# Kernel optimization log

Hardware: AMD Instinct MI355X
Metric: run time of the kernel (lower is better)

## Reference

```python
import jax, jax.numpy as jnp
import numpy as np

N = 50_000        # nodes
E = 1_600_000     # edges (avg degree 32)
H = 64            # hidden_channels
DEPTH = 3         # -> 2*DEPTH mid conv layers


def setup_inputs() -> dict:
    key = jax.random.key(0)
    ks = jax.random.split(key, 8)
    x = jax.random.normal(ks[0], (N, 1), dtype=jnp.float32)
    edge_index = jax.random.randint(ks[1], (2, E), 0, N, dtype=jnp.int32)
    s = 0.1  # small init scale
    W_in = s * jax.random.normal(ks[2], (2 * 1 + 1, H), dtype=jnp.float32)
    b_in = jnp.zeros((H,), jnp.float32)
    W_mid = s * jax.random.normal(ks[3], (2 * DEPTH, 2 * H + 1, H), dtype=jnp.float32)
    b_mid = jnp.zeros((2 * DEPTH, H), jnp.float32)
    W_out = s * jax.random.normal(ks[4], (2 * H + 1, 1), dtype=jnp.float32)
    b_out = jnp.zeros((1,), jnp.float32)
    return {"x": x, "edge_index": edge_index, "W_in": W_in, "b_in": b_in,
            "W_mid": W_mid, "b_mid": b_mid, "W_out": W_out, "b_out": b_out}


def _conv(x, src, dst, sign, inv_deg, W, b):
    """Directional_EdgeConv: mean_{j->i} Linear([x_i, x_j - x_i, sign(j-i)])."""
    x_i = x[dst]                                   # [E, F] target feats
    x_j = x[src]                                   # [E, F] source feats
    feat = jnp.concatenate([x_i, x_j - x_i, sign], axis=-1)  # [E, 2F+1]
    msg = feat @ W + b                             # [E, out]
    agg = jax.ops.segment_sum(msg, dst, num_segments=x.shape[0])  # [N, out]
    return agg * inv_deg                           # mean aggregation


def reference(x, edge_index, W_in, b_in, W_mid, b_mid, W_out, b_out):
    src = edge_index[0]
    dst = edge_index[1]
    # vectorized replacement of the per-edge Python sign loop
    sign = jnp.sign((src - dst).astype(x.dtype))[:, None]        # [E, 1]
    deg = jax.ops.segment_sum(jnp.ones((src.shape[0],), x.dtype), dst,
                              num_segments=x.shape[0])
    inv_deg = (1.0 / jnp.maximum(deg, 1.0))[:, None]             # [N, 1]

    x2 = _conv(x, src, dst, sign, inv_deg, W_in, b_in)
    for l in range(DEPTH):
        x1 = jax.nn.leaky_relu(
            _conv(x2, src, dst, sign, inv_deg, W_mid[2 * l], b_mid[2 * l]))
        x2 = jax.nn.leaky_relu(
            _conv(x1, src, dst, sign, inv_deg, W_mid[2 * l + 1], b_mid[2 * l + 1]) + x2)
    return _conv(x2, src, dst, sign, inv_deg, W_out, b_out) + x
```

## Files before the change

### kernel.cpp

```cpp
#include <hip/hip_runtime.h>
#include <hip/hip_fp16.h>

#define HDIM 64
#define NEG_SLOPE 0.01f
#define CAPB 8192
#define BCAP 6144

typedef _Float16 half8 __attribute__((ext_vector_type(8)));
typedef float f32x4 __attribute__((ext_vector_type(4)));

static __device__ __forceinline__ float h_lo(unsigned d) {
    return __half2float(__ushort_as_half((unsigned short)(d & 0xffffu)));
}
static __device__ __forceinline__ float h_hi(unsigned d) {
    return __half2float(__ushort_as_half((unsigned short)(d >> 16)));
}
static __device__ __forceinline__ unsigned packh(float a, float b) {
    unsigned short ra = __half_as_ushort(__float2half(a));
    unsigned short rb = __half_as_ushort(__float2half(b));
    return ((unsigned)rb << 16) | (unsigned)ra;
}
static __device__ __forceinline__ half8 u4h(uint4 v) {
    union { uint4 u; half8 h; } x; x.u = v; return x.h;
}
static __device__ __forceinline__ __half2 uh2(unsigned u) {
    union { unsigned u; __half2 h; } x; x.u = u; return x.h;
}

__global__ void k_setup(int ptotal, const float* __restrict__ W_mid,
                        unsigned short* __restrict__ WTh,
                        int NB, int* gcur, int N, unsigned* xAP, unsigned* xBP) {
    int i = blockIdx.x * blockDim.x + threadIdx.x;
    if (i < ptotal) {
        int l = i >> 13;
        int rem = i & 8191;
        int h = rem >> 7;
        int k = rem & 127;
        const float* W = W_mid + (size_t)l * 129 * 64;
        float v = W[k * 64 + h] - ((k < 64) ? W[(64 + k) * 64 + h] : 0.f);
        WTh[i] = __half_as_ushort(__float2half(v));
    }
    if (i < NB) gcur[i] = i * CAPB;
    if (i < 32) xAP[(size_t)N * 32 + i] = 0u;
    else if (i < 64) xBP[(size_t)N * 32 + (i - 32)] = 0u;
}

__global__ __launch_bounds__(1024) void k_bucket(
        int E, const int* __restrict__ src, const int* __restrict__ dst,
        int* gcur, unsigned* __restrict__ bucketed, int NB) {
    __shared__ int lh[512];
    __shared__ int lbase[512];
    int t = threadIdx.x;
    int e0 = blockIdx.x * 2048;
    if (t < 512) lh[t] = 0;
    __syncthreads();
    int e1 = e0 + t, e2 = e0 + 1024 + t;
    int d1 = (e1 < E) ? dst[e1] : -1;
    int d2 = (e2 < E) ? dst[e2] : -1;
    if (d1 >= 0) atomicAdd(&lh[((unsigned)d1) >> 7], 1);
    if (d2 >= 0) atomicAdd(&lh[((unsigned)d2) >> 7], 1);
    __syncthreads();
    if (t < NB) {
        int c = lh[t];
        lbase[t] = (c > 0) ? atomicAdd(&gcur[t], c) : 0;
        lh[t] = 0;
    }
    __syncthreads();
    int s1 = (e1 < E) ? src[e1] : 0;
    int s2 = (e2 < E) ? src[e2] : 0;
    if (d1 >= 0) {
        int b = ((unsigned)d1) >> 7;
        int r = atomicAdd(&lh[b], 1);
        int pos = lbase[b] + r;
        if (pos < (b + 1) * CAPB)
            bucketed[pos] = ((unsigned)d1 << 16) | (unsigned)s1;
    }
    if (d2 >= 0) {
        int b = ((unsigned)d2) >> 7;
        int r = atomicAdd(&lh[b], 1);
        int pos = lbase[b] + r;
        if (pos < (b + 1) * CAPB)
            bucketed[pos] = ((unsigned)d2 << 16) | (unsigned)s2;
    }
}

__global__ void k_bktscan(int NB, int N, const int* __restrict__ gcur,
                          int* gstart, int* rowptr) {
    __shared__ int sd[512];
    int t = threadIdx.x;
    int c = (t < NB) ? min(gcur[t] - t * CAPB, CAPB) : 0;
    sd[t] = c;
    __syncthreads();
    int x = c;
    for (int s = 1; s < 512; s <<= 1) {
        int p = (t >= s) ? sd[t - s] : 0;
        __syncthreads();
        x += p;
        sd[t] = x;
        __syncthreads();
    }
    if (t < NB) gstart[t] = x - c;
    if (t == NB - 1) {
        gstart[NB] = x;
        rowptr[N] = x;
    }
}

__global__ void k_csr(int N, const unsigned* __restrict__ bucketed, const int* __restrict__ gcur,
                      const int* __restrict__ gstart, unsigned short* __restrict__ csr,
                      unsigned short* __restrict__ pcsr,
                      int* __restrict__ rowptr, float* __restrict__ ssinv) {
    __shared__ unsigned st[BCAP];
    __shared__ int hist[128], cur[128], excl[128], sgp[128];
    int b = blockIdx.x, t = threadIdx.x;
    int n0 = b << 7;
    int nn = min(128, N - n0);
    int cnt = min(gcur[b] - b * CAPB, CAPB);
    int base = gstart[b];
    if (t < 128) { hist[t] = 0; sgp[t] = 0; }
    unsigned sent = ((unsigned)N << 16) | (unsigned)N;
    unsigned* pb32 = (unsigned*)(pcsr + ((size_t)b << 13));
    for (int i = t; i < 4096; i += 256) pb32[i] = sent;
    __syncthreads();
    bool single = (cnt <= BCAP);
    for (int off = 0; off < cnt; off += BCAP) {
        int bs = min(BCAP, cnt - off);
        for (int i = t; i < bs; i += 256) {
            unsigned w = bucketed[b * CAPB + off + i];
            if (single) st[i] = w;
            int d = (int)(w >> 16);
            int s = (int)(w & 0xffffu);
            int dl = d - n0;
            atomicAdd(&hist[dl], 1);
            atomicAdd(&sgp[dl], ((s < d) ? 1024 : 0) + ((s == d) ? 1 : 0));
        }
    }
    __syncthreads();
    int deg_t = (t < 128) ? hist[t] : 0;
    int x = deg_t;
    for (int s = 1; s < 128; s <<= 1) {
        int p = (t < 128 && t >= s) ? hist[t - s] : 0;
        __syncthreads();
        if (t < 128) { x += p; hist[t] = x; }
        __syncthreads();
    }
    if (t < 128) {
        int ex = hist[t] - deg_t;
        excl[t] = ex;
        cur[t] = ex;
        if (t < nn) {
            rowptr[n0 + t] = base + ex;
            int sg = sgp[t];
            int lt = sg >> 10, eq = sg & 1023;
            float ss = (float)(deg_t - eq - 2 * lt);
            ssinv[n0 + t] = (deg_t > 0) ? ss / (float)deg_t : 0.f;
        }
    }
    __syncthreads();
    for (int off = 0; off < cnt; off += BCAP) {
        int bs = min(BCAP, cnt - off);
        if (!single) {
            for (int i = t; i < bs; i += 256) st[i] = bucketed[b * CAPB + off + i];
            __syncthreads();
        }
        for (int i = t; i < bs; i += 256) {
            unsigned w = st[i];
            int dl = (int)(w >> 16) - n0;
            unsigned short sval = (unsigned short)(w & 0xffffu);
            int p = atomicAdd(&cur[dl], 1);
            csr[base + p] = sval;
            int r = p - excl[dl];
            if (r < 64) pcsr[((size_t)(n0 + dl) << 6) + r] = sval;
        }
        if (!single) __syncthreads();
    }
}

__global__ void k_in(int N, const float* __restrict__ x0,
                     const int* __restrict__ rowptr, const unsigned short* __restrict__ csr,
                     const float* __restrict__ ssinv,
                     const float* __restrict__ W_in, const float* __restrict__ b_in,
                     unsigned* __restrict__ xoutP) {
    int wid = blockIdx.x * (blockDim.x >> 6) + (threadIdx.x >> 6);
    int lane = threadIdx.x & 63;
    if (wid >= N) return;
    int beg = rowptr[wid], end = rowptr[wid + 1];
    int deg = end - beg;
    float s = 0.f;
    for (int e = beg + lane; e < end; e += 64) s += x0[csr[e]];
    for (int m = 32; m >= 1; m >>= 1) s += __shfl_xor(s, m, 64);
    float invd = 1.f / (float)max(deg, 1);
    float mean = s * invd;
    float xi = x0[wid];
    float w1 = W_in[lane], w2 = W_in[64 + lane], w3 = W_in[128 + lane];
    float y = xi * (w1 - w2) + mean * w2 + ssinv[wid] * w3 + b_in[lane];
    if (deg == 0) y = 0.f;
    float ylo = __shfl(y, (2 * lane) & 63, 64);
    float yhi = __shfl(y, (2 * lane + 1) & 63, 64);
    unsigned pkd = packh(ylo, yhi);
    if (lane < 32) xoutP[(size_t)wid * 32 + lane] = pkd;
}

static __device__ __forceinline__ void chunk_acc(
        const uint4* __restrict__ xin16, int sv, int base, int sub, int lq,
        __half2& c0, __half2& c1, __half2& c2, __half2& c3) {
    int s0 = __shfl(sv, base + sub, 64);
    int s1 = __shfl(sv, base + 8 + sub, 64);
    int s2 = __shfl(sv, base + 16 + sub, 64);
    int s3 = __shfl(sv, base + 24 + sub, 64);
    uint4 d0 = xin16[(size_t)s0 * 8 + lq];
    uint4 d1 = xin16[(size_t)s1 * 8 + lq];
    uint4 d2 = xin16[(size_t)s2 * 8 + lq];
    uint4 d3 = xin16[(size_t)s3 * 8 + lq];
    c0 = __hadd2(c0, __hadd2(__hadd2(uh2(d0.x), uh2(d1.x)), __hadd2(uh2(d2.x), uh2(d3.x))));
    c1 = __hadd2(c1, __hadd2(__hadd2(uh2(d0.y), uh2(d1.y)), __hadd2(uh2(d2.y), uh2(d3.y))));
    c2 = __hadd2(c2, __hadd2(__hadd2(uh2(d0.z), uh2(d1.z)), __hadd2(uh2(d2.z), uh2(d3.z))));
    c3 = __hadd2(c3, __hadd2(__hadd2(uh2(d0.w), uh2(d1.w)), __hadd2(uh2(d2.w), uh2(d3.w))));
}

static __device__ __forceinline__ void slow_gather(
        const uint4* __restrict__ xin16, const unsigned short* __restrict__ csr,
        int beg, int end, int N, int lane, int sub, int lq, float* a) {
#pragma unroll
    for (int j = 0; j < 8; ++j) a[j] = 0.f;
    for (int tb = beg; tb < end; tb += 64) {
        int cnt = min(64, end - tb);
        int sv = (lane < cnt) ? (int)csr[tb + lane] : N;
        int ng = (cnt + 7) >> 3;
        for (int g = 0; g < ng; ++g) {
            int si = __shfl(sv, (g << 3) + sub, 64);
            uint4 d = xin16[(size_t)si * 8 + lq];
            a[0] += h_lo(d.x); a[1] += h_hi(d.x);
            a[2] += h_lo(d.y); a[3] += h_hi(d.y);
            a[4] += h_lo(d.z); a[5] += h_hi(d.z);
            a[6] += h_lo(d.w); a[7] += h_hi(d.w);
        }
    }
#pragma unroll
    for (int m = 8; m <= 32; m <<= 1) {
#pragma unroll
        for (int j = 0; j < 8; ++j) a[j] += __shfl_xor(a[j], m, 64);
    }
}

template <bool RES, bool TOUT>
__global__ __launch_bounds__(256) void k_layer(
        int N, const unsigned* __restrict__ xinP,
        const unsigned* __restrict__ xresP, unsigned* __restrict__ xoutP,
        const int* __restrict__ rowptr, const unsigned short* __restrict__ csr,
        const unsigned short* __restrict__ pcsr,
        const float* __restrict__ ssinv,
        const unsigned short* __restrict__ WThl,
        const float* __restrict__ W3, const float* __restrict__ bias,
        const float* __restrict__ Wt, float* __restrict__ tvec) {
    __shared__ unsigned Ald[16 * 64];
    __shared__ float Cld[16 * 64];
    __shared__ int sdeg[16];
    __shared__ float sss[16];

    int t = threadIdx.x;
    int lane = t & 63;
    int wv = t >> 6;
    int n0 = blockIdx.x << 4;
    int kg = lane >> 4;

    int cb = (wv << 4) + (lane & 15);
    const uint4* wp = (const uint4*)WThl;
    uint4 b0 = wp[cb * 16 + kg + 0];
    uint4 b1 = wp[cb * 16 + kg + 4];
    uint4 b2 = wp[cb * 16 + kg + 8];
    uint4 b3 = wp[cb * 16 + kg + 12];

    const uint4* xin16 = (const uint4*)xinP;
    int sub = lane >> 3;
    int lq = lane & 7;
    int ndb = wv << 2;

    int svp[4];
#pragma unroll
    for (int q = 0; q < 4; ++q)
        svp[q] = (int)pcsr[((size_t)(n0 + ndb + q) << 6) + lane];

#pragma unroll
    for (int qp = 0; qp < 2; ++qp) {
        int ndA = ndb + (qp << 1);
        int ndB = ndA + 1;
        int nodeA = n0 + ndA, nodeB = n0 + ndB;
        int ncA = min(nodeA, N - 1), ncB = min(nodeB, N - 1);
        int begA = __builtin_amdgcn_readfirstlane(rowptr[ncA]);
        int endA = __builtin_amdgcn_readfirstlane(rowptr[ncA + 1]);
        int begB = __builtin_amdgcn_readfirstlane(rowptr[ncB]);
        int endB = __builtin_amdgcn_readfirstlane(rowptr[ncB + 1]);
        int degA = (nodeA < N) ? (endA - begA) : 0;
        int degB = (nodeB < N) ? (endB - begB) : 0;
        float ssvA = ssinv[ncA];
        float ssvB = ssinv[ncB];
        uint4 xiA = make_uint4(0u, 0u, 0u, 0u), xiB = make_uint4(0u, 0u, 0u, 0u);
        if (lane < 8) {
            xiA = xin16[(size_t)ncA * 8 + lane];
            xiB = xin16[(size_t)ncB * 8 + lane];
        }
        uint4 mvA, mvB;
        if (max(degA, degB) <= 64) {
            __half2 z = uh2(0u);
            __half2 cA0 = z, cA1 = z, cA2 = z, cA3 = z;
            __half2 cB0 = z, cB1 = z, cB2 = z, cB3 = z;
            int svA = svp[qp << 1], svB = svp[(qp << 1) + 1];
            chunk_acc(xin16, svA, 0, sub, lq, cA0, cA1, cA2, cA3);
            chunk_acc(xin16, svB, 0, sub, lq, cB0, cB1, cB2, cB3);
            if (degA > 32) chunk_acc(xin16, svA, 32, sub, lq, cA0, cA1, cA2, cA3);
            if (degB > 32) chunk_acc(xin16, svB, 32, sub, lq, cB0, cB1, cB2, cB3);
#pragma unroll
            for (int m = 8; m <= 32; m <<= 1) {
                cA0 = __hadd2(cA0, uh2((unsigned)__shfl_xor((int)*(unsigned*)&cA0, m, 64)));
                cA1 = __hadd2(cA1, uh2((unsigned)__shfl_xor((int)*(unsigned*)&cA1, m, 64)));
                cA2 = __hadd2(cA2, uh2((unsigned)__shfl_xor((int)*(unsigned*)&cA2, m, 64)));
                cA3 = __hadd2(cA3, uh2((unsigned)__shfl_xor((int)*(unsigned*)&cA3, m, 64)));
                cB0 = __hadd2(cB0, uh2((unsigned)__shfl_xor((int)*(unsigned*)&cB0, m, 64)));
                cB1 = __hadd2(cB1, uh2((unsigned)__shfl_xor((int)*(unsigned*)&cB1, m, 64)));
                cB2 = __hadd2(cB2, uh2((unsigned)__shfl_xor((int)*(unsigned*)&cB2, m, 64)));
                cB3 = __hadd2(cB3, uh2((unsigned)__shfl_xor((int)*(unsigned*)&cB3, m, 64)));
            }
            float idA = 1.f / (float)max(degA, 1);
            float idB = 1.f / (float)max(degB, 1);
            mvA.x = packh(__half2float(__low2half(cA0)) * idA, __half2float(__high2half(cA0)) * idA);
            mvA.y = packh(__half2float(__low2half(cA1)) * idA, __half2float(__high2half(cA1)) * idA);
            mvA.z = packh(__half2float(__low2half(cA2)) * idA, __half2float(__high2half(cA2)) * idA);
            mvA.w = packh(__half2float(__low2half(cA3)) * idA, __half2float(__high2half(cA3)) * idA);
            mvB.x = packh(__half2float(__low2half(cB0)) * idB, __half2float(__high2half(cB0)) * idB);
            mvB.y = packh(__half2float(__low2half(cB1)) * idB, __half2float(__high2half(cB1)) * idB);
            mvB.z = packh(__half2float(__low2half(cB2)) * idB, __half2float(__high2half(cB2)) * idB);
            mvB.w = packh(__half2float(__low2half(cB3)) * idB, __half2float(__high2half(cB3)) * idB);
        } else {
            float aA[8], aB[8];
            slow_gather(xin16, csr, begA, endA, N, lane, sub, lq, aA);
            slow_gather(xin16, csr, begB, endB, N, lane, sub, lq, aB);
            float idA = 1.f / (float)max(degA, 1);
            float idB = 1.f / (float)max(degB, 1);
            mvA.x = packh(aA[0] * idA, aA[1] * idA);
            mvA.y = packh(aA[2] * idA, aA[3] * idA);
            mvA.z = packh(aA[4] * idA, aA[5] * idA);
            mvA.w = packh(aA[6] * idA, aA[7] * idA);
            mvB.x = packh(aB[0] * idB, aB[1] * idB);
            mvB.y = packh(aB[2] * idB, aB[3] * idB);
            mvB.z = packh(aB[4] * idB, aB[5] * idB);
            mvB.w = packh(aB[6] * idB, aB[7] * idB);
        }
        if (lane < 8) {
            int gxA = lane ^ (ndA & 7), gmA = (8 + lane) ^ (ndA & 7);
            int gxB = lane ^ (ndB & 7), gmB = (8 + lane) ^ (ndB & 7);
            ((uint4*)Ald)[ndA * 16 + gxA] = xiA;
            ((uint4*)Ald)[ndA * 16 + gmA] = mvA;
            ((uint4*)Ald)[ndB * 16 + gxB] = xiB;
            ((uint4*)Ald)[ndB * 16 + gmB] = mvB;
        }
        if (lane == 0) {
            sdeg[ndA] = degA; sss[ndA] = ssvA;
            sdeg[ndB] = degB; sss[ndB] = ssvB;
        }
    }
    __syncthreads();

    int r = lane & 15;
    const uint4* ap = (const uint4*)Ald;
    int rx = (r & 7);
    uint4 fa0 = ap[r * 16 + ((0 + kg) ^ rx)];
    uint4 fa1 = ap[r * 16 + ((4 + kg) ^ rx)];
    uint4 fa2 = ap[r * 16 + ((8 + kg) ^ rx)];
    uint4 fa3 = ap[r * 16 + ((12 + kg) ^ rx)];
    f32x4 acc = {0.f, 0.f, 0.f, 0.f};
    acc = __builtin_amdgcn_mfma_f32_16x16x32_f16(u4h(fa0), u4h(b0), acc, 0, 0, 0);
    acc = __builtin_amdgcn_mfma_f32_16x16x32_f16(u4h(fa1), u4h(b1), acc, 0, 0, 0);
    acc = __builtin_amdgcn_mfma_f32_16x16x32_f16(u4h(fa2), u4h(b2), acc, 0, 0, 0);
    acc = __builtin_amdgcn_mfma_f32_16x16x32_f16(u4h(fa3), u4h(b3), acc, 0, 0, 0);
#pragma unroll
    for (int reg = 0; reg < 4; ++reg)
        Cld[(kg * 4 + reg) * 64 + (wv << 4) + r] = acc[reg];
    __syncthreads();

    int nd = t >> 4;
    int node = n0 + nd;
    if (node < N) {
        int dg = sdeg[nd];
        float ss = sss[nd];
        float tp = 0.f;
#pragma unroll
        for (int jj = 0; jj < 2; ++jj) {
            int j = (t & 15) + jj * 16;
            float y0 = Cld[nd * 64 + 2 * j];
            float y1 = Cld[nd * 64 + 2 * j + 1];
            float2 w3 = ((const float2*)W3)[j];
            float2 bb = ((const float2*)bias)[j];
            y0 += ss * w3.x + bb.x;
            y1 += ss * w3.y + bb.y;
            if (dg == 0) { y0 = 0.f; y1 = 0.f; }
            if (RES) {
                unsigned rw = xresP[(size_t)node * 32 + j];
                y0 += h_lo(rw);
                y1 += h_hi(rw);
            }
            y0 = (y0 > 0.f) ? y0 : NEG_SLOPE * y0;
            y1 = (y1 > 0.f) ? y1 : NEG_SLOPE * y1;
            if (TOUT) {
                float2 wt = ((const float2*)Wt)[j];
                tp += y0 * wt.x + y1 * wt.y;
            }
            xoutP[(size_t)node * 32 + j] = packh(y0, y1);
        }
        if (TOUT) {
            tp += __shfl_xor(tp, 1, 64);
            tp += __shfl_xor(tp, 2, 64);
            tp += __shfl_xor(tp, 4, 64);
            tp += __shfl_xor(tp, 8, 64);
            if ((t & 15) == 0) tvec[node] = tp;
        }
    }
}

__global__ void k_out(int N, const unsigned* __restrict__ xAP, const float* __restrict__ x0,
                      const int* __restrict__ rowptr, const unsigned short* __restrict__ csr,
                      const float* __restrict__ ssinv, const float* __restrict__ t,
                      const float* __restrict__ W_out, const float* __restrict__ b_out,
                      float* __restrict__ out) {
    int wid = blockIdx.x * (blockDim.x >> 6) + (threadIdx.x >> 6);
    int lane = threadIdx.x & 63;
    if (wid >= N) return;
    int beg = rowptr[wid], end = rowptr[wid + 1];
    int deg = end - beg;
    float s = 0.f;
    for (int e = beg + lane; e < end; e += 64) s += t[csr[e]];
    unsigned xw = xAP[(size_t)wid * 32 + (lane >> 1)];
    float xf = (lane & 1) ? h_hi(xw) : h_lo(xw);
    float p = xf * (W_out[lane] - W_out[64 + lane]);
    for (int m = 32; m >= 1; m >>= 1) {
        s += __shfl_xor(s, m, 64);
        p += __shfl_xor(p, m, 64);
    }
    float invd = 1.f / (float)max(deg, 1);
    float y = p + s * invd + ssinv[wid] * W_out[128] + b_out[0];
    if (deg == 0) y = 0.f;
    if (lane == 0) out[wid] = y + x0[wid];
}

static inline size_t align16(size_t x) { return (x + 15) & ~(size_t)15; }

extern "C" void kernel_launch(void* const* d_in, const int* in_sizes, int n_in,
                              void* d_out, int out_size, void* d_ws, size_t ws_size,
                              hipStream_t stream) {
    const float* x0    = (const float*)d_in[0];
    const int*   ei    = (const int*)d_in[1];
    const float* W_in  = (const float*)d_in[2];
    const float* b_in  = (const float*)d_in[3];
    const float* W_mid = (const float*)d_in[4];
    const float* b_mid = (const float*)d_in[5];
    const float* W_out = (const float*)d_in[6];
    const float* b_out = (const float*)d_in[7];
    float* out = (float*)d_out;

    const int N = in_sizes[0];
    const int E = in_sizes[1] / 2;
    const int L = in_sizes[4] / (129 * 64);
    const int NB = (N + 127) >> 7;
    const int* src = ei;
    const int* dst = ei + E;

    char* p = (char*)d_ws;
    unsigned short* WTh = (unsigned short*)p; p += align16((size_t)L * 64 * 128 * 2);
    unsigned* xAP = (unsigned*)p; p += align16((size_t)(N + 1) * 32 * 4);
    unsigned* xBP = (unsigned*)p; p += align16((size_t)(N + 1) * 32 * 4);
    unsigned* bucketed = (unsigned*)p; p += align16((size_t)NB * CAPB * 4);
    unsigned short* csr = (unsigned short*)p; p += align16((size_t)E * 2);
    unsigned short* pcsr = (unsigned short*)p; p += align16((size_t)NB * 8192 * 2);
    int* gcur          = (int*)p; p += align16((size_t)(NB + 1) * 4);
    int* gstart        = (int*)p; p += align16((size_t)(NB + 1) * 4);
    int* rowptr        = (int*)p; p += align16((size_t)(N + 1) * 4);
    float* ssinv       = (float*)p; p += align16((size_t)N * 4);
    float* t           = (float*)p; p += align16((size_t)N * 4);

    const int nb_w4 = (N + 3) / 4;
    const int nb_bkt = (E + 2047) / 2048;
    const int ptotal = L * 64 * 128;
    const int nb_lay = (N + 15) / 16;

    k_setup<<<(ptotal + 255) / 256, 256, 0, stream>>>(ptotal, W_mid, WTh, NB, gcur, N, xAP, xBP);
    k_bucket<<<nb_bkt, 1024, 0, stream>>>(E, src, dst, gcur, bucketed, NB);
    k_bktscan<<<1, 512, 0, stream>>>(NB, N, gcur, gstart, rowptr);
    k_csr<<<NB, 256, 0, stream>>>(N, bucketed, gcur, gstart, csr, pcsr, rowptr, ssinv);

    k_in<<<nb_w4, 256, 0, stream>>>(N, x0, rowptr, csr, ssinv, W_in, b_in, xAP);

    for (int l = 0; l < L / 2; ++l) {
        bool last = (l == L / 2 - 1);
        const unsigned short* Wa = WTh + (size_t)(2 * l) * 64 * 128;
        const unsigned short* Wb = WTh + (size_t)(2 * l + 1) * 64 * 128;
        const float* W3a = W_mid + (size_t)(2 * l) * 129 * 64 + 128 * 64;
        const float* W3b = W_mid + (size_t)(2 * l + 1) * 129 * 64 + 128 * 64;

        k_layer<false, false><<<nb_lay, 256, 0, stream>>>(
            N, xAP, nullptr, xBP, rowptr, csr, pcsr, ssinv,
            Wa, W3a, b_mid + (size_t)(2 * l) * HDIM, nullptr, nullptr);
        if (!last) {
            k_layer<true, false><<<nb_lay, 256, 0, stream>>>(
                N, xBP, xAP, xAP, rowptr, csr, pcsr, ssinv,
                Wb, W3b, b_mid + (size_t)(2 * l + 1) * HDIM, nullptr, nullptr);
        } else {
            k_layer<true, true><<<nb_lay, 256, 0, stream>>>(
                N, xBP, xAP, xAP, rowptr, csr, pcsr, ssinv,
                Wb, W3b, b_mid + (size_t)(2 * l + 1) * HDIM, W_out + 64, t);
        }
    }

    k_out<<<nb_w4, 256, 0, stream>>>(N, xAP, x0, rowptr, csr, ssinv, t,
                                     W_out, b_out, out);
}
```

Before: 254.7 us.

## Batch neighbor gathers across four nodes per wave and use padded CSR in output

The layer kernel's gather stage now handles all four nodes of a wave together. It issues sixteen independent row loads up front before accumulating, instead of processing nodes in pairs. The degree>32 tail is split into 8-neighbor steps, and the slow path runs only for the specific nodes above 64. The output kernel reads the padded per-node CSR with a single load per lane when degree ≤64, relying on a zeroed sentinel t[N]. The goal is more memory-level parallelism, at the cost of higher register pressure from the 16 in-flight uint4 loads.

```diff
diff --git a/kernel.cpp b/kernel.cpp
--- a/kernel.cpp
+++ b/kernel.cpp
@@ -26,10 +26,14 @@
 static __device__ __forceinline__ __half2 uh2(unsigned u) {
     union { unsigned u; __half2 h; } x; x.u = u; return x.h;
 }
+static __device__ __forceinline__ unsigned h2u(__half2 h) {
+    union { __half2 h; unsigned u; } x; x.h = h; return x.u;
+}
 
 __global__ void k_setup(int ptotal, const float* __restrict__ W_mid,
                         unsigned short* __restrict__ WTh,
-                        int NB, int* gcur, int N, unsigned* xAP, unsigned* xBP) {
+                        int NB, int* gcur, int N, unsigned* xAP, unsigned* xBP,
+                        float* tvec) {
     int i = blockIdx.x * blockDim.x + threadIdx.x;
     if (i < ptotal) {
         int l = i >> 13;
@@ -43,6 +47,7 @@
     if (i < NB) gcur[i] = i * CAPB;
     if (i < 32) xAP[(size_t)N * 32 + i] = 0u;
     else if (i < 64) xBP[(size_t)N * 32 + (i - 32)] = 0u;
+    else if (i == 64) tvec[N] = 0.f;
 }
 
 __global__ __launch_bounds__(1024) void k_bucket(
@@ -201,23 +206,6 @@
     if (lane < 32) xoutP[(size_t)wid * 32 + lane] = pkd;
 }
 
-static __device__ __forceinline__ void chunk_acc(
-        const uint4* __restrict__ xin16, int sv, int base, int sub, int lq,
-        __half2& c0, __half2& c1, __half2& c2, __half2& c3) {
-    int s0 = __shfl(sv, base + sub, 64);
-    int s1 = __shfl(sv, base + 8 + sub, 64);
-    int s2 = __shfl(sv, base + 16 + sub, 64);
-    int s3 = __shfl(sv, base + 24 + sub, 64);
-    uint4 d0 = xin16[(size_t)s0 * 8 + lq];
-    uint4 d1 = xin16[(size_t)s1 * 8 + lq];
-    uint4 d2 = xin16[(size_t)s2 * 8 + lq];
-    uint4 d3 = xin16[(size_t)s3 * 8 + lq];
-    c0 = __hadd2(c0, __hadd2(__hadd2(uh2(d0.x), uh2(d1.x)), __hadd2(uh2(d2.x), uh2(d3.x))));
-    c1 = __hadd2(c1, __hadd2(__hadd2(uh2(d0.y), uh2(d1.y)), __hadd2(uh2(d2.y), uh2(d3.y))));
-    c2 = __hadd2(c2, __hadd2(__hadd2(uh2(d0.z), uh2(d1.z)), __hadd2(uh2(d2.z), uh2(d3.z))));
-    c3 = __hadd2(c3, __hadd2(__hadd2(uh2(d0.w), uh2(d1.w)), __hadd2(uh2(d2.w), uh2(d3.w))));
-}
-
 static __device__ __forceinline__ void slow_gather(
         const uint4* __restrict__ xin16, const unsigned short* __restrict__ csr,
         int beg, int end, int N, int lane, int sub, int lq, float* a) {
@@ -276,88 +264,122 @@
     int lq = lane & 7;
     int ndb = wv << 2;
 
-    int svp[4];
+    int svp[4], degq[4], begq[4], endq[4];
+    float ssq[4];
+#pragma unroll
+    for (int q = 0; q < 4; ++q) {
+        int node = n0 + ndb + q;
+        int nc = min(node, N - 1);
+        svp[q] = (int)pcsr[((size_t)(n0 + ndb + q) << 6) + lane];
+        int bg = __builtin_amdgcn_readfirstlane(rowptr[nc]);
+        int en = __builtin_amdgcn_readfirstlane(rowptr[nc + 1]);
+        begq[q] = bg; endq[q] = en;
+        degq[q] = (node < N) ? (en - bg) : 0;
+        ssq[q] = ssinv[nc];
+    }
+
+    __half2 z = uh2(0u);
+    __half2 c[4][4];
 #pragma unroll
     for (int q = 0; q < 4; ++q)
-        svp[q] = (int)pcsr[((size_t)(n0 + ndb + q) << 6) + lane];
-
-#pragma unroll
-    for (int qp = 0; qp < 2; ++qp) {
-        int ndA = ndb + (qp << 1);
-        int ndB = ndA + 1;
-        int nodeA = n0 + ndA, nodeB = n0 + ndB;
-        int ncA = min(nodeA, N - 1), ncB = min(nodeB, N - 1);
-        int begA = __builtin_amdgcn_readfirstlane(rowptr[ncA]);
-        int endA = __builtin_amdgcn_readfirstlane(rowptr[ncA + 1]);
-        int begB = __builtin_amdgcn_readfirstlane(rowptr[ncB]);
-        int endB = __builtin_amdgcn_readfirstlane(rowptr[ncB + 1]);
-        int degA = (nodeA < N) ? (endA - begA) : 0;
-        int degB = (nodeB < N) ? (endB - begB) : 0;
-        float ssvA = ssinv[ncA];
-        float ssvB = ssinv[ncB];
-        uint4 xiA = make_uint4(0u, 0u, 0u, 0u), xiB = make_uint4(0u, 0u, 0u, 0u);
+#pragma unroll
+        for (int j = 0; j < 4; ++j) c[q][j] = z;
+
+    int sidx[16];
+#pragma unroll
+    for (int q = 0; q < 4; ++q)
+#pragma unroll
+        for (int g = 0; g < 4; ++g)
+            sidx[q * 4 + g] = __shfl(svp[q], (g << 3) + sub, 64);
+    uint4 dv[16];
+#pragma unroll
+    for (int i = 0; i < 16; ++i)
+        dv[i] = xin16[(size_t)sidx[i] * 8 + lq];
+#pragma unroll
+    for (int q = 0; q < 4; ++q) {
+#pragma unroll
+        for (int g = 0; g < 4; ++g) {
+            uint4 d = dv[q * 4 + g];
+            c[q][0] = __hadd2(c[q][0], uh2(d.x));
+            c[q][1] = __hadd2(c[q][1], uh2(d.y));
+            c[q][2] = __hadd2(c[q][2], uh2(d.z));
+            c[q][3] = __hadd2(c[q][3], uh2(d.w));
+        }
+    }
+
+#pragma unroll
+    for (int q = 0; q < 4; ++q) {
+        if (degq[q] > 32) {
+            int s4 = __shfl(svp[q], 32 + sub, 64);
+            int s5 = __shfl(svp[q], 40 + sub, 64);
+            uint4 d4 = xin16[(size_t)s4 * 8 + lq];
+            uint4 d5 = xin16[(size_t)s5 * 8 + lq];
+            c[q][0] = __hadd2(c[q][0], __hadd2(uh2(d4.x), uh2(d5.x)));
+            c[q][1] = __hadd2(c[q][1], __hadd2(uh2(d4.y), uh2(d5.y)));
+            c[q][2] = __hadd2(c[q][2], __hadd2(uh2(d4.z), uh2(d5.z)));
+            c[q][3] = __hadd2(c[q][3], __hadd2(uh2(d4.w), uh2(d5.w)));
+            if (degq[q] > 48) {
+                int s6 = __shfl(svp[q], 48 + sub, 64);
+                int s7 = __shfl(svp[q], 56 + sub, 64);
+                uint4 d6 = xin16[(size_t)s6 * 8 + lq];
+                uint4 d7 = xin16[(size_t)s7 * 8 + lq];
+                c[q][0] = __hadd2(c[q][0], __hadd2(uh2(d6.x), uh2(d7.x)));
+                c[q][1] = __hadd2(c[q][1], __hadd2(uh2(d6.y), uh2(d7.y)));
+                c[q][2] = __hadd2(c[q][2], __hadd2(uh2(d6.z), uh2(d7.z)));
+                c[q][3] = __hadd2(c[q][3], __hadd2(uh2(d6.w), uh2(d7.w)));
+            }
+        }
+    }
+
+#pragma unroll
+    for (int m = 8; m <= 32; m <<= 1) {
+#pragma unroll
+        for (int q = 0; q < 4; ++q)
+#pragma unroll
+            for (int j = 0; j < 4; ++j)
+                c[q][j] = __hadd2(c[q][j], uh2((unsigned)__shfl_xor((int)h2u(c[q][j]), m, 64)));
+    }
+
+    uint4 mv[4];
+#pragma unroll
+    for (int q = 0; q < 4; ++q) {
+        float id = 1.f / (float)max(degq[q], 1);
+        mv[q].x = packh(__half2float(__low2half(c[q][0])) * id, __half2float(__high2half(c[q][0])) * id);
+        mv[q].y = packh(__half2float(__low2half(c[q][1])) * id, __half2float(__high2half(c[q][1])) * id);
+        mv[q].z = packh(__half2float(__low2half(c[q][2])) * id, __half2float(__high2half(c[q][2])) * id);
+        mv[q].w = packh(__half2float(__low2half(c[q][3])) * id, __half2float(__high2half(c[q][3])) * id);
+    }
+
+    int mx = max(max(degq[0], degq[1]), max(degq[2], degq[3]));
+    if (mx > 64) {
+#pragma unroll
+        for (int q = 0; q < 4; ++q) {
+            if (degq[q] > 64) {
+                float a[8];
+                slow_gather(xin16, csr, begq[q], endq[q], N, lane, sub, lq, a);
+                float id = 1.f / (float)degq[q];
+                mv[q].x = packh(a[0] * id, a[1] * id);
+                mv[q].y = packh(a[2] * id, a[3] * id);
+                mv[q].z = packh(a[4] * id, a[5] * id);
+                mv[q].w = packh(a[6] * id, a[7] * id);
+            }
+        }
+    }
+
+#pragma unroll
+    for (int q = 0; q < 4; ++q) {
+        int nd = ndb + q;
+        int node = n0 + nd;
+        int nc = min(node, N - 1);
+        uint4 xi4 = make_uint4(0u, 0u, 0u, 0u);
+        if (lane < 8 && node < N) xi4 = xin16[(size_t)nc * 8 + lane];
         if (lane < 8) {
-            xiA = xin16[(size_t)ncA * 8 + lane];
-            xiB = xin16[(size_t)ncB * 8 + lane];
-        }
-        uint4 mvA, mvB;
-        if (max(degA, degB) <= 64) {
-            __half2 z = uh2(0u);
-            __half2 cA0 = z, cA1 = z, cA2 = z, cA3 = z;
-            __half2 cB0 = z, cB1 = z, cB2 = z, cB3 = z;
-            int svA = svp[qp << 1], svB = svp[(qp << 1) + 1];
-            chunk_acc(xin16, svA, 0, sub, lq, cA0, cA1, cA2, cA3);
-            chunk_acc(xin16, svB, 0, sub, lq, cB0, cB1, cB2, cB3);
-            if (degA > 32) chunk_acc(xin16, svA, 32, sub, lq, cA0, cA1, cA2, cA3);
-            if (degB > 32) chunk_acc(xin16, svB, 32, sub, lq, cB0, cB1, cB2, cB3);
-#pragma unroll
-            for (int m = 8; m <= 32; m <<= 1) {
-                cA0 = __hadd2(cA0, uh2((unsigned)__shfl_xor((int)*(unsigned*)&cA0, m, 64)));
-                cA1 = __hadd2(cA1, uh2((unsigned)__shfl_xor((int)*(unsigned*)&cA1, m, 64)));
-                cA2 = __hadd2(cA2, uh2((unsigned)__shfl_xor((int)*(unsigned*)&cA2, m, 64)));
-                cA3 = __hadd2(cA3, uh2((unsigned)__shfl_xor((int)*(unsigned*)&cA3, m, 64)));
-                cB0 = __hadd2(cB0, uh2((unsigned)__shfl_xor((int)*(unsigned*)&cB0, m, 64)));
-                cB1 = __hadd2(cB1, uh2((unsigned)__shfl_xor((int)*(unsigned*)&cB1, m, 64)));
-                cB2 = __hadd2(cB2, uh2((unsigned)__shfl_xor((int)*(unsigned*)&cB2, m, 64)));
-                cB3 = __hadd2(cB3, uh2((unsigned)__shfl_xor((int)*(unsigned*)&cB3, m, 64)));
-            }
-            float idA = 1.f / (float)max(degA, 1);
-            float idB = 1.f / (float)max(degB, 1);
-            mvA.x = packh(__half2float(__low2half(cA0)) * idA, __half2float(__high2half(cA0)) * idA);
-            mvA.y = packh(__half2float(__low2half(cA1)) * idA, __half2float(__high2half(cA1)) * idA);
-            mvA.z = packh(__half2float(__low2half(cA2)) * idA, __half2float(__high2half(cA2)) * idA);
-            mvA.w = packh(__half2float(__low2half(cA3)) * idA, __half2float(__high2half(cA3)) * idA);
-            mvB.x = packh(__half2float(__low2half(cB0)) * idB, __half2float(__high2half(cB0)) * idB);
-            mvB.y = packh(__half2float(__low2half(cB1)) * idB, __half2float(__high2half(cB1)) * idB);
-            mvB.z = packh(__half2float(__low2half(cB2)) * idB, __half2float(__high2half(cB2)) * idB);
-            mvB.w = packh(__half2float(__low2half(cB3)) * idB, __half2float(__high2half(cB3)) * idB);
-        } else {
-            float aA[8], aB[8];
-            slow_gather(xin16, csr, begA, endA, N, lane, sub, lq, aA);
-            slow_gather(xin16, csr, begB, endB, N, lane, sub, lq, aB);
-            float idA = 1.f / (float)max(degA, 1);
-            float idB = 1.f / (float)max(degB, 1);
-            mvA.x = packh(aA[0] * idA, aA[1] * idA);
-            mvA.y = packh(aA[2] * idA, aA[3] * idA);
-            mvA.z = packh(aA[4] * idA, aA[5] * idA);
-            mvA.w = packh(aA[6] * idA, aA[7] * idA);
-            mvB.x = packh(aB[0] * idB, aB[1] * idB);
-            mvB.y = packh(aB[2] * idB, aB[3] * idB);
-            mvB.z = packh(aB[4] * idB, aB[5] * idB);
-            mvB.w = packh(aB[6] * idB, aB[7] * idB);
-        }
-        if (lane < 8) {
-            int gxA = lane ^ (ndA & 7), gmA = (8 + lane) ^ (ndA & 7);
-            int gxB = lane ^ (ndB & 7), gmB = (8 + lane) ^ (ndB & 7);
-            ((uint4*)Ald)[ndA * 16 + gxA] = xiA;
-            ((uint4*)Ald)[ndA * 16 + gmA] = mvA;
-            ((uint4*)Ald)[ndB * 16 + gxB] = xiB;
-            ((uint4*)Ald)[ndB * 16 + gmB] = mvB;
-        }
-        if (lane == 0) {
-            sdeg[ndA] = degA; sss[ndA] = ssvA;
-            sdeg[ndB] = degB; sss[ndB] = ssvB;
-        }
+            int gx = lane ^ (nd & 7);
+            int gm = (8 + lane) ^ (nd & 7);
+            ((uint4*)Ald)[nd * 16 + gx] = xi4;
+            ((uint4*)Ald)[nd * 16 + gm] = mv[q];
+        }
+        if (lane == 0) { sdeg[nd] = degq[q]; sss[nd] = ssq[q]; }
     }
     __syncthreads();
 
@@ -419,6 +441,7 @@
 
 __global__ void k_out(int N, const unsigned* __restrict__ xAP, const float* __restrict__ x0,
                       const int* __restrict__ rowptr, const unsigned short* __restrict__ csr,
+                      const unsigned short* __restrict__ pcsr,
                       const float* __restrict__ ssinv, const float* __restrict__ t,
                       const float* __restrict__ W_out, const float* __restrict__ b_out,
                       float* __restrict__ out) {
@@ -427,8 +450,14 @@
     if (wid >= N) return;
     int beg = rowptr[wid], end = rowptr[wid + 1];
     int deg = end - beg;
-    float s = 0.f;
-    for (int e = beg + lane; e < end; e += 64) s += t[csr[e]];
+    float s;
+    if (deg <= 64) {
+        int sl = (int)pcsr[((size_t)wid << 6) + lane];
+        s = t[sl];
+    } else {
+        s = 0.f;
+        for (int e = beg + lane; e < end; e += 64) s += t[csr[e]];
+    }
     unsigned xw = xAP[(size_t)wid * 32 + (lane >> 1)];
     float xf = (lane & 1) ? h_hi(xw) : h_lo(xw);
     float p = xf * (W_out[lane] - W_out[64 + lane]);
@@ -475,14 +504,14 @@
     int* gstart        = (int*)p; p += align16((size_t)(NB + 1) * 4);
     int* rowptr        = (int*)p; p += align16((size_t)(N + 1) * 4);
     float* ssinv       = (float*)p; p += align16((size_t)N * 4);
-    float* t           = (float*)p; p += align16((size_t)N * 4);
+    float* t           = (float*)p; p += align16((size_t)(N + 1) * 4);
 
     const int nb_w4 = (N + 3) / 4;
     const int nb_bkt = (E + 2047) / 2048;
     const int ptotal = L * 64 * 128;
     const int nb_lay = (N + 15) / 16;
 
-    k_setup<<<(ptotal + 255) / 256, 256, 0, stream>>>(ptotal, W_mid, WTh, NB, gcur, N, xAP, xBP);
+    k_setup<<<(ptotal + 255) / 256, 256, 0, stream>>>(ptotal, W_mid, WTh, NB, gcur, N, xAP, xBP, t);
     k_bucket<<<nb_bkt, 1024, 0, stream>>>(E, src, dst, gcur, bucketed, NB);
     k_bktscan<<<1, 512, 0, stream>>>(NB, N, gcur, gstart, rowptr);
     k_csr<<<NB, 256, 0, stream>>>(N, bucketed, gcur, gstart, csr, pcsr, rowptr, ssinv);
@@ -510,6 +539,6 @@
         }
     }
 
-    k_out<<<nb_w4, 256, 0, stream>>>(N, xAP, x0, rowptr, csr, ssinv, t,
+    k_out<<<nb_w4, 256, 0, stream>>>(N, xAP, x0, rowptr, csr, pcsr, ssinv, t,
                                      W_out, b_out, out);
 }
```

New measurement: 290.6 us. 14.1% more time.
